# Performance work log

Measured on AMD Instinct MI355X. Metric: run time of the kernel, lower is better.

Reference implementation:

```python
import jax, jax.numpy as jnp
import numpy as np

IN_DIM, HID, OUT_DIM, PRED_LEN = 33, 64, 2, 25
B, P, T = 1024, 22, 20
EPS = 1e-5


def _lstm_step(Wih, Whh, b, h, c, xt):
    # PyTorch gate order: i, f, g, o
    gates = xt @ Wih.T + h @ Whh.T + b
    i, f, g, o = jnp.split(gates, 4, axis=-1)
    c_new = jax.nn.sigmoid(f) * c + jax.nn.sigmoid(i) * jnp.tanh(g)
    h_new = jax.nn.sigmoid(o) * jnp.tanh(c_new)
    return h_new, c_new


def setup_inputs() -> dict:
    key = jax.random.key(0)
    ks = jax.random.split(key, 20)
    s = 0.1
    inp = {
        "x": jax.random.normal(ks[0], (B, P, T, IN_DIM), dtype=jnp.float32),
        "enc_Wih": jax.random.normal(ks[1], (4 * HID, IN_DIM)) * s,
        "enc_Whh": jax.random.normal(ks[2], (4 * HID, HID)) * s,
        "enc_bih": jax.random.normal(ks[3], (4 * HID,)) * s,
        "enc_bhh": jax.random.normal(ks[4], (4 * HID,)) * s,
        "q_W": jax.random.normal(ks[5], (HID, HID)) * s,
        "q_b": jax.random.normal(ks[6], (HID,)) * s,
        "k_W": jax.random.normal(ks[7], (HID, HID)) * s,
        "k_b": jax.random.normal(ks[8], (HID,)) * s,
        "v_W": jax.random.normal(ks[9], (HID, HID)) * s,
        "v_b": jax.random.normal(ks[10], (HID,)) * s,
        "ln_g": jnp.ones((HID,), jnp.float32),
        "ln_b": jnp.zeros((HID,), jnp.float32),
        "dec_Wih": jax.random.normal(ks[11], (4 * HID, OUT_DIM)) * s,
        "dec_Whh": jax.random.normal(ks[12], (4 * HID, HID)) * s,
        "dec_bih": jax.random.normal(ks[13], (4 * HID,)) * s,
        "dec_bhh": jax.random.normal(ks[14], (4 * HID,)) * s,
        "fc_W": jax.random.normal(ks[15], (OUT_DIM, HID)) * s,
        "fc_b": jax.random.normal(ks[16], (OUT_DIM,)) * s,
    }
    return inp


def reference(x, enc_Wih, enc_Whh, enc_bih, enc_bhh, q_W, q_b, k_W, k_b,
              v_W, v_b, ln_g, ln_b, dec_Wih, dec_Whh, dec_bih, dec_bhh,
              fc_W, fc_b):
    b, p, t, d = x.shape
    n = b * p
    xf = x.reshape(n, t, d)

    # ----- encoder LSTM over history -----
    b_enc = enc_bih + enc_bhh
    def enc_step(carry, xt):
        h, c = carry
        h, c = _lstm_step(enc_Wih, enc_Whh, b_enc, h, c, xt)
        return (h, c), None
    h0 = jnp.zeros((n, HID), x.dtype)
    (hn, cn), _ = jax.lax.scan(enc_step, (h0, h0), xf.transpose(1, 0, 2))

    # ----- interaction GNN (self-attention over players) -----
    last_hidden = hn.reshape(b, p, HID)
    Q = last_hidden @ q_W.T + q_b
    K = last_hidden @ k_W.T + k_b
    V = last_hidden @ v_W.T + v_b
    scores = jnp.einsum('bph,bqh->bpq', Q, K) / jnp.sqrt(jnp.float32(HID))
    attn = jax.nn.softmax(scores, axis=-1)
    ctx = jnp.einsum('bpq,bqh->bph', attn, V)

    # ----- layernorm(residual) -----
    y = last_hidden + ctx
    mu = y.mean(-1, keepdims=True)
    var = y.var(-1, keepdims=True)
    y = (y - mu) / jnp.sqrt(var + EPS) * ln_g + ln_b

    b_dec = dec_bih + dec_bhh
    def dec_step(carry, _):
        h, c, inp = carry
        h, c = _lstm_step(dec_Wih, dec_Whh, b_dec, h, c, inp)
        pred = h @ fc_W.T + fc_b
        return (h, c, pred), pred
    inp0 = xf[:, -1, :OUT_DIM]
    _, preds = jax.lax.scan(dec_step, (y.reshape(n, HID), cn, inp0),
                            None, length=PRED_LEN)  # [PRED_LEN, n, 2]
    return preds.transpose(1, 0, 2).reshape(b, p, PRED_LEN, OUT_DIM)
```

## Files before the change

kernel.cpp:

```cpp
#include <hip/hip_runtime.h>

typedef short short8 __attribute__((ext_vector_type(8)));
typedef float f32x4 __attribute__((ext_vector_type(4)));

#define IN_DIM   33
#define HID      64
#define OUT_DIM  2
#define PRED_LEN 25
#define NB       1024
#define NP       22
#define NT       20
#define EPS      1e-5f

#define SWZ(s,k) (((s) << 7) + ((k) ^ (((s) & 7) << 3)))

__device__ __forceinline__ float fast_rcp(float x){ return __builtin_amdgcn_rcpf(x); }
__device__ __forceinline__ float sigm(float x){ return fast_rcp(1.0f + __expf(-x)); }
__device__ __forceinline__ float tanhf_(float x){ float e = __expf(2.0f*x); return 1.0f - 2.0f*fast_rcp(e + 1.0f); }
__device__ __forceinline__ unsigned short bf_hi(float f){
    unsigned u = __float_as_uint(f);
    return (unsigned short)((u + 0x7fffu + ((u >> 16) & 1u)) >> 16);
}
__device__ __forceinline__ float bf_f(unsigned short h){ return __uint_as_float(((unsigned)h) << 16); }
__device__ __forceinline__ unsigned cvt_pk_bf16(float a, float b){
    unsigned r;
    asm("v_cvt_pk_bf16_f32 %0, %1, %2" : "=v"(r) : "v"(a), "v"(b));
    return r;
}

__global__ __launch_bounds__(256, 2) void nfl_mfma(
    const float* __restrict__ x,
    const float* __restrict__ enc_Wih, const float* __restrict__ enc_Whh,
    const float* __restrict__ enc_bih, const float* __restrict__ enc_bhh,
    const float* __restrict__ q_W, const float* __restrict__ q_b,
    const float* __restrict__ k_W, const float* __restrict__ k_b,
    const float* __restrict__ v_W, const float* __restrict__ v_b,
    const float* __restrict__ ln_g, const float* __restrict__ ln_b,
    const float* __restrict__ dec_Wih, const float* __restrict__ dec_Whh,
    const float* __restrict__ dec_bih, const float* __restrict__ dec_bhh,
    const float* __restrict__ fc_W, const float* __restrict__ fc_b,
    float* __restrict__ out)
{
    __shared__ __align__(16) unsigned char arena[32*128*2*2];
    __shared__ float sh_q [NP*66];
    __shared__ float sh_f [NP*66];
    __shared__ float sh_sc[NP*24];
    __shared__ float sh_p0[32];
    __shared__ float sh_p1[32];
    __shared__ float sh_mu[NP];
    __shared__ float sh_rs[NP];

    unsigned short* shA_hi = (unsigned short*)arena;
    unsigned short* shA_lo = (unsigned short*)(arena + 8192);
    float* sh_k = (float*)arena;
    float* sh_v = (float*)(arena + 8192);

    const int tid  = threadIdx.x;
    const int w    = tid >> 6;
    const int ln   = tid & 63;
    const int lo15 = ln & 15;
    const int qq   = ln >> 4;
    const int jh   = 16*w + lo15;
    const int b    = blockIdx.x;
    const float* xb = x + (size_t)b * NP*NT*IN_DIM;

    short8 eBh[4][4], eBl[4][4];
    float bias_e[4];
    #pragma unroll
    for (int nt = 0; nt < 4; nt++){
        int g = 16*w + 64*nt + lo15;
        bias_e[nt] = enc_bih[g] + enc_bhh[g];
        #pragma unroll
        for (int kt = 0; kt < 4; kt++){
            #pragma unroll
            for (int e = 0; e < 8; e++){
                int k = 32*kt + 8*qq + e;
                float v;
                if (k < HID) v = enc_Whh[g*HID + k];
                else { int d = k - HID; v = (d < IN_DIM) ? enc_Wih[g*IN_DIM + d] : 0.0f; }
                unsigned short h = bf_hi(v);
                eBh[nt][kt][e] = (short)h;
                eBl[nt][kt][e] = (short)bf_hi(v - bf_f(h));
            }
        }
    }

    for (int i = tid; i < 32*128; i += 256) ((unsigned*)arena)[i] = 0;

    float cst[2][4] = {{0,0,0,0},{0,0,0,0}};
    __syncthreads();

    auto stage_x = [&](int t){
        for (int i = tid; i < NP*IN_DIM; i += 256){
            int s = i / IN_DIM, d = i - s * IN_DIM;
            float v = xb[(s*NT + t)*IN_DIM + d];
            unsigned short h = bf_hi(v);
            int idx = SWZ(s, HID + d);
            shA_hi[idx] = h; shA_lo[idx] = bf_hi(v - bf_f(h));
        }
    };

    auto nonlin_store = [&](f32x4 (&acc)[2][4], bool save_f){
        #pragma unroll
        for (int m = 0; m < 2; m++){
            #pragma unroll
            for (int jp = 0; jp < 2; jp++){
                const int j0 = 2*jp;
                float hh0, hh1;
                {
                    float gi=acc[m][0][j0], gf=acc[m][1][j0], gg=acc[m][2][j0], go=acc[m][3][j0];
                    float c = sigm(gf)*cst[m][j0] + sigm(gi)*tanhf_(gg);
                    cst[m][j0] = c;
                    hh0 = sigm(go)*tanhf_(c);
                }
                {
                    float gi=acc[m][0][j0+1], gf=acc[m][1][j0+1], gg=acc[m][2][j0+1], go=acc[m][3][j0+1];
                    float c = sigm(gf)*cst[m][j0+1] + sigm(gi)*tanhf_(gg);
                    cst[m][j0+1] = c;
                    hh1 = sigm(go)*tanhf_(c);
                }
                unsigned hp = cvt_pk_bf16(hh0, hh1);
                float r0 = hh0 - __uint_as_float(hp << 16);
                float r1 = hh1 - __uint_as_float(hp & 0xffff0000u);
                unsigned lp = cvt_pk_bf16(r0, r1);
                const int s0 = 16*m + 4*qq + j0;
                if (s0 < NP){
                    int i0 = SWZ(s0, jh);
                    shA_hi[i0] = (unsigned short)hp;
                    shA_lo[i0] = (unsigned short)lp;
                    if (save_f) sh_f[s0*66 + jh] = hh0;
                }
                if (s0 + 1 < NP){
                    int i1 = SWZ(s0 + 1, jh);
                    shA_hi[i1] = (unsigned short)(hp >> 16);
                    shA_lo[i1] = (unsigned short)(lp >> 16);
                    if (save_f) sh_f[(s0+1)*66 + jh] = hh1;
                }
            }
        }
    };

    stage_x(0);
    __syncthreads();
    for (int t = 0; t < NT; t++){
        f32x4 acc[2][4];
        #pragma unroll
        for (int m = 0; m < 2; m++)
            #pragma unroll
            for (int nt = 0; nt < 4; nt++){
                float bb = bias_e[nt];
                acc[m][nt][0]=bb; acc[m][nt][1]=bb; acc[m][nt][2]=bb; acc[m][nt][3]=bb;
            }
        #pragma unroll
        for (int kt = 0; kt < 4; kt++){
            #pragma unroll
            for (int m = 0; m < 2; m++){
                int idx = SWZ(16*m + lo15, 32*kt + 8*qq);
                short8 ah = *reinterpret_cast<const short8*>(&shA_hi[idx]);
                short8 al = *reinterpret_cast<const short8*>(&shA_lo[idx]);
                #pragma unroll
                for (int nt = 0; nt < 4; nt++){
                    acc[m][nt] = __builtin_amdgcn_mfma_f32_16x16x32_bf16(ah, eBh[nt][kt], acc[m][nt], 0,0,0);
                    acc[m][nt] = __builtin_amdgcn_mfma_f32_16x16x32_bf16(al, eBh[nt][kt], acc[m][nt], 0,0,0);
                    acc[m][nt] = __builtin_amdgcn_mfma_f32_16x16x32_bf16(ah, eBl[nt][kt], acc[m][nt], 0,0,0);
                }
            }
        }
        __syncthreads();
        if (t + 1 < NT) stage_x(t + 1);
        nonlin_store(acc, t == NT-1);
        __syncthreads();
    }

    {
        short8 qBh[3][2], qBl[3][2];
        float qb3[3];
        #pragma unroll
        for (int mat = 0; mat < 3; mat++){
            const float* W  = (mat==0) ? q_W : (mat==1) ? k_W : v_W;
            const float* bb = (mat==0) ? q_b : (mat==1) ? k_b : v_b;
            qb3[mat] = bb[jh];
            #pragma unroll
            for (int kt = 0; kt < 2; kt++){
                #pragma unroll
                for (int e = 0; e < 8; e++){
                    int k = 32*kt + 8*qq + e;
                    float v = W[jh*HID + k];
                    unsigned short h = bf_hi(v);
                    qBh[mat][kt][e] = (short)h;
                    qBl[mat][kt][e] = (short)bf_hi(v - bf_f(h));
                }
            }
        }
        f32x4 qacc[3][2];
        #pragma unroll
        for (int mat = 0; mat < 3; mat++)
            #pragma unroll
            for (int m = 0; m < 2; m++){
                float bb = qb3[mat];
                qacc[mat][m][0]=bb; qacc[mat][m][1]=bb; qacc[mat][m][2]=bb; qacc[mat][m][3]=bb;
            }
        #pragma unroll
        for (int kt = 0; kt < 2; kt++){
            #pragma unroll
            for (int m = 0; m < 2; m++){
                int idx = SWZ(16*m + lo15, 32*kt + 8*qq);
                short8 ah = *reinterpret_cast<const short8*>(&shA_hi[idx]);
                short8 al = *reinterpret_cast<const short8*>(&shA_lo[idx]);
                #pragma unroll
                for (int mat = 0; mat < 3; mat++){
                    qacc[mat][m] = __builtin_amdgcn_mfma_f32_16x16x32_bf16(ah, qBh[mat][kt], qacc[mat][m], 0,0,0);
                    qacc[mat][m] = __builtin_amdgcn_mfma_f32_16x16x32_bf16(al, qBh[mat][kt], qacc[mat][m], 0,0,0);
                    qacc[mat][m] = __builtin_amdgcn_mfma_f32_16x16x32_bf16(ah, qBl[mat][kt], qacc[mat][m], 0,0,0);
                }
            }
        }
        __syncthreads();
        #pragma unroll
        for (int mat = 0; mat < 3; mat++){
            float* dst = (mat==0) ? sh_q : (mat==1) ? sh_k : sh_v;
            #pragma unroll
            for (int m = 0; m < 2; m++)
                #pragma unroll
                for (int j = 0; j < 4; j++){
                    int s = 16*m + 4*qq + j;
                    if (s < NP) dst[s*66 + jh] = qacc[mat][m][j];
                }
        }
    }
    __syncthreads();

    for (int i = tid; i < NP*NP; i += 256){
        int p = i / NP, q = i - p*NP;
        float acc = 0.0f;
        #pragma unroll
        for (int k = 0; k < HID; k++) acc = fmaf(sh_q[p*66 + k], sh_k[q*66 + k], acc);
        sh_sc[p*24 + q] = acc * 0.125f;
    }
    __syncthreads();

    if (tid < NP){
        float m = -1e30f;
        for (int q = 0; q < NP; q++) m = fmaxf(m, sh_sc[tid*24 + q]);
        float sum = 0.0f;
        for (int q = 0; q < NP; q++){ float e = __expf(sh_sc[tid*24 + q] - m); sh_sc[tid*24 + q] = e; sum += e; }
        float inv = fast_rcp(sum);
        for (int q = 0; q < NP; q++) sh_sc[tid*24 + q] *= inv;
    }
    __syncthreads();

    for (int i = tid; i < NP*HID; i += 256){
        int s = i >> 6, j = i & 63;
        float acc = 0.0f;
        #pragma unroll
        for (int q = 0; q < NP; q++) acc = fmaf(sh_sc[s*24 + q], sh_v[q*66 + j], acc);
        sh_f[s*66 + j] += acc;
    }
    __syncthreads();

    if (tid < NP){
        float mu = 0.0f;
        for (int j = 0; j < HID; j++) mu += sh_f[tid*66 + j];
        mu *= (1.0f/HID);
        float var = 0.0f;
        for (int j = 0; j < HID; j++){ float d = sh_f[tid*66 + j] - mu; var += d*d; }
        sh_mu[tid] = mu;
        sh_rs[tid] = rsqrtf(var*(1.0f/HID) + EPS);
    }
    __syncthreads();

    for (int i = tid; i < NP*HID/2; i += 256){
        int s = i >> 5, j0 = (i & 31) << 1;
        float sc = sh_rs[s], mu = sh_mu[s];
        float v0 = (sh_f[s*66 + j0]   - mu) * sc * ln_g[j0]   + ln_b[j0];
        float v1 = (sh_f[s*66 + j0+1] - mu) * sc * ln_g[j0+1] + ln_b[j0+1];
        unsigned hp = cvt_pk_bf16(v0, v1);
        float r0 = v0 - __uint_as_float(hp << 16);
        float r1 = v1 - __uint_as_float(hp & 0xffff0000u);
        unsigned lp = cvt_pk_bf16(r0, r1);
        int idx = SWZ(s, j0);
        *(unsigned*)&shA_hi[idx] = hp;
        *(unsigned*)&shA_lo[idx] = lp;
    }
    if (tid < 32){
        float v0 = 0.0f, v1 = 0.0f;
        if (tid < NP){
            v0 = xb[(tid*NT + NT-1)*IN_DIM + 0];
            v1 = xb[(tid*NT + NT-1)*IN_DIM + 1];
        }
        sh_p0[tid] = v0; sh_p1[tid] = v1;
    }

    short8 dBh[4][2], dBl[4][2];
    float bias_d[4], wd0[4], wd1[4];
    #pragma unroll
    for (int nt = 0; nt < 4; nt++){
        int g = 16*w + 64*nt + lo15;
        bias_d[nt] = dec_bih[g] + dec_bhh[g];
        wd0[nt] = dec_Wih[g*OUT_DIM + 0];
        wd1[nt] = dec_Wih[g*OUT_DIM + 1];
        #pragma unroll
        for (int kt = 0; kt < 2; kt++){
            #pragma unroll
            for (int e = 0; e < 8; e++){
                int k = 32*kt + 8*qq + e;
                float v = dec_Whh[g*HID + k];
                unsigned short h = bf_hi(v);
                dBh[nt][kt][e] = (short)h;
                dBl[nt][kt][e] = (short)bf_hi(v - bf_f(h));
            }
        }
    }
    const int fitem = tid >> 2, fq = tid & 3, fs = fitem >> 1, fo = fitem & 1;
    float fcw[16]; float fcb = 0.0f;
    if (tid < 176){
        #pragma unroll
        for (int jj = 0; jj < 16; jj++) fcw[jj] = fc_W[fo*HID + 16*fq + jj];
        fcb = fc_b[fo];
    }
    float* outb = out + (size_t)b * NP * PRED_LEN * OUT_DIM;
    __syncthreads();

    for (int t = 0; t < PRED_LEN; t++){
        f32x4 acc[2][4];
        #pragma unroll
        for (int m = 0; m < 2; m++){
            #pragma unroll
            for (int j = 0; j < 4; j++){
                int s = 16*m + 4*qq + j;
                float p0 = sh_p0[s], p1 = sh_p1[s];
                #pragma unroll
                for (int nt = 0; nt < 4; nt++)
                    acc[m][nt][j] = bias_d[nt] + wd0[nt]*p0 + wd1[nt]*p1;
            }
        }
        #pragma unroll
        for (int kt = 0; kt < 2; kt++){
            #pragma unroll
            for (int m = 0; m < 2; m++){
                int idx = SWZ(16*m + lo15, 32*kt + 8*qq);
                short8 ah = *reinterpret_cast<const short8*>(&shA_hi[idx]);
                short8 al = *reinterpret_cast<const short8*>(&shA_lo[idx]);
                #pragma unroll
                for (int nt = 0; nt < 4; nt++){
                    acc[m][nt] = __builtin_amdgcn_mfma_f32_16x16x32_bf16(ah, dBh[nt][kt], acc[m][nt], 0,0,0);
                    acc[m][nt] = __builtin_amdgcn_mfma_f32_16x16x32_bf16(al, dBh[nt][kt], acc[m][nt], 0,0,0);
                    acc[m][nt] = __builtin_amdgcn_mfma_f32_16x16x32_bf16(ah, dBl[nt][kt], acc[m][nt], 0,0,0);
                }
            }
        }
        __syncthreads();

        nonlin_store(acc, false);
        __syncthreads();

        if (tid < 176){
            int idx0 = SWZ(fs, 16*fq);
            int idx1 = SWZ(fs, 16*fq + 8);
            short8 h0h = *reinterpret_cast<const short8*>(&shA_hi[idx0]);
            short8 h0l = *reinterpret_cast<const short8*>(&shA_lo[idx0]);
            short8 h1h = *reinterpret_cast<const short8*>(&shA_hi[idx1]);
            short8 h1l = *reinterpret_cast<const short8*>(&shA_lo[idx1]);
            float part = 0.0f;
            #pragma unroll
            for (int e = 0; e < 8; e++){
                part = fmaf(bf_f((unsigned short)h0h[e]) + bf_f((unsigned short)h0l[e]), fcw[e],     part);
                part = fmaf(bf_f((unsigned short)h1h[e]) + bf_f((unsigned short)h1l[e]), fcw[8 + e], part);
            }
            part += __shfl_xor(part, 1);
            part += __shfl_xor(part, 2);
            if (fq == 0){
                float pred = part + fcb;
                outb[(fs*PRED_LEN + t)*OUT_DIM + fo] = pred;
                if (fo == 0) sh_p0[fs] = pred; else sh_p1[fs] = pred;
            }
        }
        __syncthreads();
    }
}

extern "C" void kernel_launch(void* const* d_in, const int* in_sizes, int n_in,
                              void* d_out, int out_size, void* d_ws, size_t ws_size,
                              hipStream_t stream) {
    const float* x        = (const float*)d_in[0];
    const float* enc_Wih  = (const float*)d_in[1];
    const float* enc_Whh  = (const float*)d_in[2];
    const float* enc_bih  = (const float*)d_in[3];
    const float* enc_bhh  = (const float*)d_in[4];
    const float* q_W      = (const float*)d_in[5];
    const float* q_b      = (const float*)d_in[6];
    const float* k_W      = (const float*)d_in[7];
    const float* k_b      = (const float*)d_in[8];
    const float* v_W      = (const float*)d_in[9];
    const float* v_b      = (const float*)d_in[10];
    const float* ln_g     = (const float*)d_in[11];
    const float* ln_b     = (const float*)d_in[12];
    const float* dec_Wih  = (const float*)d_in[13];
    const float* dec_Whh  = (const float*)d_in[14];
    const float* dec_bih  = (const float*)d_in[15];
    const float* dec_bhh  = (const float*)d_in[16];
    const float* fc_W     = (const float*)d_in[17];
    const float* fc_b     = (const float*)d_in[18];
    float* out = (float*)d_out;

    nfl_mfma<<<dim3(NB), dim3(256), 0, stream>>>(
        x, enc_Wih, enc_Whh, enc_bih, enc_bhh,
        q_W, q_b, k_W, k_b, v_W, v_b, ln_g, ln_b,
        dec_Wih, dec_Whh, dec_bih, dec_bhh, fc_W, fc_b, out);
}
```

Baseline: 385.1 us.

## Double-buffer LSTM hidden-state tiles to drop one barrier per step

Stores the bf16 hi/lo hidden-state A tiles in two ping-pong buffers, so each recurrent step reads one buffer and writes the other. This removes one __syncthreads per encoder and decoder step. The next timestep's x values are now prefetched into registers before the MFMAs and converted afterwards, hiding global load latency. Shared memory use doubles for the arena, which may affect the 2-blocks-per-CU occupancy, and it adds register pressure.

```diff
diff --git a/kernel.cpp b/kernel.cpp
--- a/kernel.cpp
+++ b/kernel.cpp
@@ -41,7 +41,7 @@
     const float* __restrict__ fc_W, const float* __restrict__ fc_b,
     float* __restrict__ out)
 {
-    __shared__ __align__(16) unsigned char arena[32*128*2*2];
+    __shared__ __align__(16) unsigned char arena[4*8192];
     __shared__ float sh_q [NP*66];
     __shared__ float sh_f [NP*66];
     __shared__ float sh_sc[NP*24];
@@ -50,10 +50,8 @@
     __shared__ float sh_mu[NP];
     __shared__ float sh_rs[NP];
 
-    unsigned short* shA_hi = (unsigned short*)arena;
-    unsigned short* shA_lo = (unsigned short*)(arena + 8192);
-    float* sh_k = (float*)arena;
-    float* sh_v = (float*)(arena + 8192);
+    float* sh_k = (float*)(arena + 16384);
+    float* sh_v = (float*)(arena + 16384 + 8192);
 
     const int tid  = threadIdx.x;
     const int w    = tid >> 6;
@@ -64,6 +62,9 @@
     const int b    = blockIdx.x;
     const float* xb = x + (size_t)b * NP*NT*IN_DIM;
 
+    auto Ahi = [&](int p){ return (unsigned short*)(arena + p*16384); };
+    auto Alo = [&](int p){ return (unsigned short*)(arena + p*16384 + 8192); };
+
     short8 eBh[4][4], eBl[4][4];
     float bias_e[4];
     #pragma unroll
@@ -85,22 +86,13 @@
         }
     }
 
-    for (int i = tid; i < 32*128; i += 256) ((unsigned*)arena)[i] = 0;
+    for (int i = tid; i < 4*2048; i += 256) ((unsigned*)arena)[i] = 0;
 
     float cst[2][4] = {{0,0,0,0},{0,0,0,0}};
     __syncthreads();
 
-    auto stage_x = [&](int t){
-        for (int i = tid; i < NP*IN_DIM; i += 256){
-            int s = i / IN_DIM, d = i - s * IN_DIM;
-            float v = xb[(s*NT + t)*IN_DIM + d];
-            unsigned short h = bf_hi(v);
-            int idx = SWZ(s, HID + d);
-            shA_hi[idx] = h; shA_lo[idx] = bf_hi(v - bf_f(h));
-        }
-    };
-
-    auto nonlin_store = [&](f32x4 (&acc)[2][4], bool save_f){
+    auto nonlin_store = [&](f32x4 (&acc)[2][4], unsigned short* wh,
+                            unsigned short* wl, bool save_f){
         #pragma unroll
         for (int m = 0; m < 2; m++){
             #pragma unroll
@@ -126,23 +118,50 @@
                 const int s0 = 16*m + 4*qq + j0;
                 if (s0 < NP){
                     int i0 = SWZ(s0, jh);
-                    shA_hi[i0] = (unsigned short)hp;
-                    shA_lo[i0] = (unsigned short)lp;
+                    wh[i0] = (unsigned short)hp;
+                    wl[i0] = (unsigned short)lp;
                     if (save_f) sh_f[s0*66 + jh] = hh0;
                 }
                 if (s0 + 1 < NP){
                     int i1 = SWZ(s0 + 1, jh);
-                    shA_hi[i1] = (unsigned short)(hp >> 16);
-                    shA_lo[i1] = (unsigned short)(lp >> 16);
+                    wh[i1] = (unsigned short)(hp >> 16);
+                    wl[i1] = (unsigned short)(lp >> 16);
                     if (save_f) sh_f[(s0+1)*66 + jh] = hh1;
                 }
             }
         }
     };
 
-    stage_x(0);
-    __syncthreads();
+    {
+        unsigned short* wh = Ahi(0); unsigned short* wl = Alo(0);
+        for (int i = tid; i < NP*IN_DIM; i += 256){
+            int s = i / IN_DIM, d = i - s * IN_DIM;
+            float v = xb[(s*NT + 0)*IN_DIM + d];
+            unsigned short h = bf_hi(v);
+            int idx = SWZ(s, HID + d);
+            wh[idx] = h; wl[idx] = bf_hi(v - bf_f(h));
+        }
+    }
+    __syncthreads();
+
     for (int t = 0; t < NT; t++){
+        const int p = t & 1;
+        unsigned short* rh = Ahi(p);     unsigned short* rl = Alo(p);
+        unsigned short* wh = Ahi(1 - p); unsigned short* wl = Alo(1 - p);
+
+        float xr[3];
+        const bool have_x = (t + 1 < NT);
+        if (have_x){
+            #pragma unroll
+            for (int sl = 0; sl < 3; sl++){
+                int i = tid + 256*sl;
+                if (i < NP*IN_DIM){
+                    int s = i / IN_DIM, d = i - s * IN_DIM;
+                    xr[sl] = xb[(s*NT + (t+1))*IN_DIM + d];
+                }
+            }
+        }
+
         f32x4 acc[2][4];
         #pragma unroll
         for (int m = 0; m < 2; m++)
@@ -156,8 +175,8 @@
             #pragma unroll
             for (int m = 0; m < 2; m++){
                 int idx = SWZ(16*m + lo15, 32*kt + 8*qq);
-                short8 ah = *reinterpret_cast<const short8*>(&shA_hi[idx]);
-                short8 al = *reinterpret_cast<const short8*>(&shA_lo[idx]);
+                short8 ah = *reinterpret_cast<const short8*>(&rh[idx]);
+                short8 al = *reinterpret_cast<const short8*>(&rl[idx]);
                 #pragma unroll
                 for (int nt = 0; nt < 4; nt++){
                     acc[m][nt] = __builtin_amdgcn_mfma_f32_16x16x32_bf16(ah, eBh[nt][kt], acc[m][nt], 0,0,0);
@@ -166,13 +185,24 @@
                 }
             }
         }
+        nonlin_store(acc, wh, wl, t == NT-1);
+        if (have_x){
+            #pragma unroll
+            for (int sl = 0; sl < 3; sl++){
+                int i = tid + 256*sl;
+                if (i < NP*IN_DIM){
+                    int s = i / IN_DIM, d = i - s * IN_DIM;
+                    unsigned short h = bf_hi(xr[sl]);
+                    int idx = SWZ(s, HID + d);
+                    wh[idx] = h; wl[idx] = bf_hi(xr[sl] - bf_f(h));
+                }
+            }
+        }
         __syncthreads();
-        if (t + 1 < NT) stage_x(t + 1);
-        nonlin_store(acc, t == NT-1);
-        __syncthreads();
     }
 
     {
+        unsigned short* rh = Ahi(0); unsigned short* rl = Alo(0);
         short8 qBh[3][2], qBl[3][2];
         float qb3[3];
         #pragma unroll
@@ -205,8 +235,8 @@
             #pragma unroll
             for (int m = 0; m < 2; m++){
                 int idx = SWZ(16*m + lo15, 32*kt + 8*qq);
-                short8 ah = *reinterpret_cast<const short8*>(&shA_hi[idx]);
-                short8 al = *reinterpret_cast<const short8*>(&shA_lo[idx]);
+                short8 ah = *reinterpret_cast<const short8*>(&rh[idx]);
+                short8 al = *reinterpret_cast<const short8*>(&rl[idx]);
                 #pragma unroll
                 for (int mat = 0; mat < 3; mat++){
                     qacc[mat][m] = __builtin_amdgcn_mfma_f32_16x16x32_bf16(ah, qBh[mat][kt], qacc[mat][m], 0,0,0);
@@ -215,7 +245,6 @@
                 }
             }
         }
-        __syncthreads();
         #pragma unroll
         for (int mat = 0; mat < 3; mat++){
             float* dst = (mat==0) ? sh_q : (mat==1) ? sh_k : sh_v;
@@ -269,18 +298,21 @@
     }
     __syncthreads();
 
-    for (int i = tid; i < NP*HID/2; i += 256){
-        int s = i >> 5, j0 = (i & 31) << 1;
-        float sc = sh_rs[s], mu = sh_mu[s];
-        float v0 = (sh_f[s*66 + j0]   - mu) * sc * ln_g[j0]   + ln_b[j0];
-        float v1 = (sh_f[s*66 + j0+1] - mu) * sc * ln_g[j0+1] + ln_b[j0+1];
-        unsigned hp = cvt_pk_bf16(v0, v1);
-        float r0 = v0 - __uint_as_float(hp << 16);
-        float r1 = v1 - __uint_as_float(hp & 0xffff0000u);
-        unsigned lp = cvt_pk_bf16(r0, r1);
-        int idx = SWZ(s, j0);
-        *(unsigned*)&shA_hi[idx] = hp;
-        *(unsigned*)&shA_lo[idx] = lp;
+    {
+        unsigned short* wh = Ahi(0); unsigned short* wl = Alo(0);
+        for (int i = tid; i < NP*HID/2; i += 256){
+            int s = i >> 5, j0 = (i & 31) << 1;
+            float sc = sh_rs[s], mu = sh_mu[s];
+            float v0 = (sh_f[s*66 + j0]   - mu) * sc * ln_g[j0]   + ln_b[j0];
+            float v1 = (sh_f[s*66 + j0+1] - mu) * sc * ln_g[j0+1] + ln_b[j0+1];
+            unsigned hp = cvt_pk_bf16(v0, v1);
+            float r0 = v0 - __uint_as_float(hp << 16);
+            float r1 = v1 - __uint_as_float(hp & 0xffff0000u);
+            unsigned lp = cvt_pk_bf16(r0, r1);
+            int idx = SWZ(s, j0);
+            *(unsigned*)&wh[idx] = hp;
+            *(unsigned*)&wl[idx] = lp;
+        }
     }
     if (tid < 32){
         float v0 = 0.0f, v1 = 0.0f;
@@ -322,6 +354,10 @@
     __syncthreads();
 
     for (int t = 0; t < PRED_LEN; t++){
+        const int p = t & 1;
+        unsigned short* rh = Ahi(p);     unsigned short* rl = Alo(p);
+        unsigned short* wh = Ahi(1 - p); unsigned short* wl = Alo(1 - p);
+
         f32x4 acc[2][4];
         #pragma unroll
         for (int m = 0; m < 2; m++){
@@ -339,8 +375,8 @@
             #pragma unroll
             for (int m = 0; m < 2; m++){
                 int idx = SWZ(16*m + lo15, 32*kt + 8*qq);
-                short8 ah = *reinterpret_cast<const short8*>(&shA_hi[idx]);
-                short8 al = *reinterpret_cast<const short8*>(&shA_lo[idx]);
+                short8 ah = *reinterpret_cast<const short8*>(&rh[idx]);
+                short8 al = *reinterpret_cast<const short8*>(&rl[idx]);
                 #pragma unroll
                 for (int nt = 0; nt < 4; nt++){
                     acc[m][nt] = __builtin_amdgcn_mfma_f32_16x16x32_bf16(ah, dBh[nt][kt], acc[m][nt], 0,0,0);
@@ -349,18 +385,16 @@
                 }
             }
         }
-        __syncthreads();
-
-        nonlin_store(acc, false);
+        nonlin_store(acc, wh, wl, false);
         __syncthreads();
 
         if (tid < 176){
             int idx0 = SWZ(fs, 16*fq);
             int idx1 = SWZ(fs, 16*fq + 8);
-            short8 h0h = *reinterpret_cast<const short8*>(&shA_hi[idx0]);
-            short8 h0l = *reinterpret_cast<const short8*>(&shA_lo[idx0]);
-            short8 h1h = *reinterpret_cast<const short8*>(&shA_hi[idx1]);
-            short8 h1l = *reinterpret_cast<const short8*>(&shA_lo[idx1]);
+            short8 h0h = *reinterpret_cast<const short8*>(&wh[idx0]);
+            short8 h0l = *reinterpret_cast<const short8*>(&wl[idx0]);
+            short8 h1h = *reinterpret_cast<const short8*>(&wh[idx1]);
+            short8 h1l = *reinterpret_cast<const short8*>(&wl[idx1]);
             float part = 0.0f;
             #pragma unroll
             for (int e = 0; e < 8; e++){
```

Measured after the change: 359.7 us. 6.6% less time.
